# Kernel optimization log

Measured on AMD Instinct MI355X. Metric: run time of the kernel, lower is better.

## Reference

```python
import jax, jax.numpy as jnp
import numpy as np

S = 64        # state_size (nodes per graph == feature width)
B = 1024      # number of graphs
N = B * S     # total nodes
DEG = 16      # avg degree
E = N * DEG   # total edges
A = 16        # attractors
EPS = 1e-5


def setup_inputs() -> dict:
    key = jax.random.key(0)
    ks = jax.random.split(key, 16)
    x = jax.random.normal(ks[0], (N, 1), dtype=jnp.float32)
    # block-diagonal batched graphs: each graph has S nodes, S*DEG edges
    epg = S * DEG
    gid = jnp.arange(E, dtype=jnp.int32) // epg
    src = gid * S + jax.random.randint(ks[1], (E,), 0, S, dtype=jnp.int32)
    dst = gid * S + jax.random.randint(ks[2], (E,), 0, S, dtype=jnp.int32)
    edge_index = jnp.stack([src, dst], axis=0)
    f32 = jnp.float32
    return {
        "x": x, "edge_index": edge_index,
        # EdgeConv MLP: Linear(2,4) -> ReLU -> Linear(4,S)
        "w1": jax.random.normal(ks[3], (2, 4), f32) * 0.5,
        "b1": jnp.zeros((4,), f32),
        "w2": jax.random.normal(ks[4], (4, S), f32) * 0.3,
        "b2": jnp.zeros((S,), f32),
        # Conv1d(S,S,3,padding=1) x2
        "conv2_w": jax.random.normal(ks[5], (S, S, 3), f32) / np.sqrt(3 * S),
        "conv2_b": jnp.zeros((S,), f32),
        "conv3_w": jax.random.normal(ks[6], (S, S, 3), f32) / np.sqrt(3 * S),
        "conv3_b": jnp.zeros((S,), f32),
        # BatchNorm affine params
        "g1": jnp.ones((S,), f32), "be1": jnp.zeros((S,), f32),
        "g2": jnp.ones((S,), f32), "be2": jnp.zeros((S,), f32),
        "g3": jnp.ones((S,), f32), "be3": jnp.zeros((S,), f32),
        # MLP tail
        "wm1": jax.random.normal(ks[7], (S * S, 256), f32) / np.sqrt(S * S),
        "bm1": jnp.zeros((256,), f32),
        "wm2": jax.random.normal(ks[8], (256, 256), f32) / 16.0,
        "bm2": jnp.zeros((256,), f32),
        "wm3": jax.random.normal(ks[9], (256, 256), f32) / 16.0,
        "bm3": jnp.zeros((256,), f32),
        "wp": jax.random.normal(ks[10], (256, A), f32) / 16.0,
        "bp": jnp.zeros((A,), f32),
    }


def _bn(h, gamma, beta, axes):
    # training-mode batch norm (biased variance), per-channel
    mean = jnp.mean(h, axis=axes, keepdims=True)
    var = jnp.mean(jnp.square(h - mean), axis=axes, keepdims=True)
    inv = jax.lax.rsqrt(var + EPS)
    sh = [1] * h.ndim
    sh[1] = -1
    return (h - mean) * inv * gamma.reshape(sh) + beta.reshape(sh)


def _conv1d(h, w, b):
    # h: [B, C, L], w: [O, I, K], padding=1 -> same length
    out = jax.lax.conv_general_dilated(
        h, w, window_strides=(1,), padding=((1, 1),),
        dimension_numbers=("NCH", "OIH", "NCH"))
    return out + b[None, :, None]


def reference(x, edge_index, w1, b1, w2, b2, conv2_w, conv2_b, conv3_w, conv3_b,
              g1, be1, g2, be2, g3, be3, wm1, bm1, wm2, bm2, wm3, bm3, wp, bp):
    src, dst = edge_index[0], edge_index[1]
    # EdgeConv (aggr='add'): nn(cat[x_i, x_j - x_i]) summed at target i
    xi = x[dst]                              # [E,1] gather
    xj = x[src]                              # [E,1] gather
    m = jnp.concatenate([xi, xj - xi], axis=-1)      # [E,2]
    m = jax.nn.relu(m @ w1 + b1)                     # [E,4]
    m = m @ w2 + b2                                   # [E,S]
    out = jax.ops.segment_sum(m, dst, num_segments=N)  # [N,S] scatter-add
    # BN1 + ReLU on [N,S] (channel dim = 1)
    out = jax.nn.relu(_bn(out, g1, be1, axes=(0,)))
    # per-graph feature map: [B, S_nodes, S_feat] -> channels-first [B,S,S]
    out = out.reshape(B, S, S).swapaxes(1, 2)
    out = jax.nn.relu(_bn(_conv1d(out, conv2_w, conv2_b), g2, be2, axes=(0, 2)))
    out = jax.nn.relu(_bn(_conv1d(out, conv3_w, conv3_b), g3, be3, axes=(0, 2)))
    out = out.reshape(B, S * S)
    out = jax.nn.relu(out @ wm1 + bm1)
    out = jax.nn.relu(out @ wm2 + bm2)
    out = jax.nn.relu(out @ wm3 + bm3)
    logits = out @ wp + bp                            # [B, A]
    return jax.nn.log_softmax(logits, axis=1)
```

## Files before the change

### kernel.cpp

```cpp
#include <hip/hip_runtime.h>
#include <cstdint>
#include <cstddef>

typedef __attribute__((ext_vector_type(8))) short short8;
typedef __attribute__((ext_vector_type(4))) float f32x4;

#define EPSV 1e-5f
#define NB 1024
#define NEDGE 1048576
#define EPG 1024
#define CNTF 65536.0f
#define REP 32

__device__ __forceinline__ ushort f2bf(float f) {
  uint u = __float_as_uint(f);
  return (ushort)((u + 0x7FFFu + ((u >> 16) & 1u)) >> 16);
}

__global__ __launch_bounds__(256) void k_prepc(
    const float* __restrict__ c2w, const float* __restrict__ c3w,
    ushort* __restrict__ cwt2, ushort* __restrict__ cwt3)
{
  const int flat = blockIdx.x * 256 + threadIdx.x;
  const int m = flat >= 12288;
  const int idx = flat - (m ? 12288 : 0);
  const float* src = m ? c3w : c2w;
  ushort* dst = m ? cwt3 : cwt2;
  const int o = idx / 192, rem = idx - o * 192;
  const int kk = rem >> 6, c = rem & 63;
  dst[idx] = f2bf(src[o * 192 + c * 3 + kk]);
}

__global__ __launch_bounds__(256) void k_edge(
    const float* __restrict__ x, const int* __restrict__ ei,
    const float* __restrict__ w1, const float* __restrict__ b1,
    const float* __restrict__ w2, const float* __restrict__ b2,
    float* __restrict__ out0, float* __restrict__ stats1)
{
  __shared__ float xs[64];
  __shared__ float aggT[4][5][72];
  __shared__ float aggC[64][8];
  __shared__ float w1s[8], b1s[4];
  __shared__ float w2s[256], b2s[64];
  __shared__ float rs[4][64], rss[4][64];
  const int tid = threadIdx.x;
  const int b = blockIdx.x;
  const int w = tid >> 6;

  if (tid < 8) w1s[tid] = w1[tid];
  if (tid < 4) b1s[tid] = b1[tid];
  if (tid < 64) { xs[tid] = x[(b << 6) + tid]; b2s[tid] = b2[tid]; }
  w2s[tid] = w2[tid];
  for (int i = tid; i < 1440; i += 256) ((float*)aggT)[i] = 0.f;
  __syncthreads();

  const int e0 = b * EPG;
  const int4 s4 = ((const int4*)(ei + e0))[tid];
  const int4 d4 = ((const int4*)(ei + NEDGE + e0))[tid];
  float* agw = &aggT[w][0][0];
  const int sls[4] = {s4.x & 63, s4.y & 63, s4.z & 63, s4.w & 63};
  const int dls[4] = {d4.x & 63, d4.y & 63, d4.z & 63, d4.w & 63};
#pragma unroll
  for (int e = 0; e < 4; ++e) {
    const int dl = dls[e];
    const float xi = xs[dl];
    const float dx = xs[sls[e]] - xi;
#pragma unroll
    for (int j = 0; j < 4; ++j) {
      float h = fmaxf(fmaf(xi, w1s[j], fmaf(dx, w1s[4 + j], b1s[j])), 0.f);
      atomicAdd(&agw[j * 72 + dl], h);
    }
    atomicAdd(&agw[4 * 72 + dl], 1.0f);
  }
  __syncthreads();

  if (tid < 64) {
    const int n = tid;
    const float a0 = aggT[0][0][n] + aggT[1][0][n] + aggT[2][0][n] + aggT[3][0][n];
    const float a1 = aggT[0][1][n] + aggT[1][1][n] + aggT[2][1][n] + aggT[3][1][n];
    const float a2 = aggT[0][2][n] + aggT[1][2][n] + aggT[2][2][n] + aggT[3][2][n];
    const float a3v = aggT[0][3][n] + aggT[1][3][n] + aggT[2][3][n] + aggT[3][3][n];
    const float dg = aggT[0][4][n] + aggT[1][4][n] + aggT[2][4][n] + aggT[3][4][n];
    *(float4*)&aggC[n][0] = make_float4(a0, a1, a2, a3v);
    aggC[n][4] = dg;
  }
  __syncthreads();

  const int c = tid & 63, qq = tid >> 6;
  const float wc0 = w2s[c], wc1 = w2s[64 + c], wc2 = w2s[128 + c], wc3 = w2s[192 + c];
  const float b2c = b2s[c];
  float s = 0.f, ss = 0.f;
  for (int n = qq; n < 64; n += 4) {
    const float4 a = *(const float4*)&aggC[n][0];
    const float dg = aggC[n][4];
    float v = a.x * wc0 + a.y * wc1 + a.z * wc2 + a.w * wc3 + dg * b2c;
    out0[(size_t)(((b << 6) + n) << 6) + c] = v;
    s += v; ss += v * v;
  }
  rs[qq][c] = s; rss[qq][c] = ss;
  __syncthreads();
  if (tid < 64) {
    float* dst = stats1 + ((b & (REP - 1)) << 7);
    atomicAdd(&dst[tid], rs[0][tid] + rs[1][tid] + rs[2][tid] + rs[3][tid]);
    atomicAdd(&dst[64 + tid], rss[0][tid] + rss[1][tid] + rss[2][tid] + rss[3][tid]);
  }
}

__global__ __launch_bounds__(256) void k_convm(
    const float* __restrict__ in,
    const float* __restrict__ stats_in,
    const float* __restrict__ gamma, const float* __restrict__ beta,
    const ushort* __restrict__ cwt, const float* __restrict__ cb,
    float* __restrict__ out,
    float* __restrict__ stats_out)
{
  __shared__ ushort As[64][200];
  __shared__ ushort Yt[66][72];
  __shared__ float aco[64], bco[64], cbs[64];
  __shared__ float ldsS[64], ldsSS[64];
  const int tid = threadIdx.x;
  const int b = blockIdx.x;

  if (tid < 64) {
    float sm = 0.f, sq = 0.f;
#pragma unroll 8
    for (int r = 0; r < REP; ++r) {
      sm += stats_in[(r << 7) + tid];
      sq += stats_in[(r << 7) + 64 + tid];
    }
    const float mean = sm * (1.0f / CNTF);
    const float var = sq * (1.0f / CNTF) - mean * mean;
    const float a = gamma[tid] * rsqrtf(var + EPSV);
    aco[tid] = a;
    bco[tid] = beta[tid] - mean * a;
    cbs[tid] = cb[tid];
    Yt[0][tid] = 0;
    Yt[65][tid] = 0;
  }
  __syncthreads();

  const size_t base = (size_t)b << 12;
  {
    const int lr = tid >> 4, c0 = (tid & 15) << 2;
#pragma unroll
    for (int i = 0; i < 4; ++i) {
      const int l = lr + (i << 4);
      const float4 v = *(const float4*)&in[base + (l << 6) + c0];
      const float4 a4 = *(const float4*)&aco[c0];
      const float4 b4 = *(const float4*)&bco[c0];
      *(ushort4*)&Yt[l + 1][c0] = make_ushort4(
          f2bf(fmaxf(fmaf(a4.x, v.x, b4.x), 0.f)),
          f2bf(fmaxf(fmaf(a4.y, v.y, b4.y), 0.f)),
          f2bf(fmaxf(fmaf(a4.z, v.z, b4.z), 0.f)),
          f2bf(fmaxf(fmaf(a4.w, v.w, b4.w), 0.f)));
    }
  }
  {
    const short8* gw = (const short8*)cwt;
#pragma unroll
    for (int i = 0; i < 6; ++i) {
      const int e8 = (i << 8) + tid;
      const int o = e8 / 24, k8 = (e8 - o * 24) << 3;
      *(short8*)&As[o][k8] = gw[e8];
    }
  }
  __syncthreads();

  const int lane = tid & 63, w = tid >> 6;
  const int lm = lane & 15, q = lane >> 4;
  f32x4 acc[4];
#pragma unroll
  for (int nt = 0; nt < 4; ++nt) acc[nt] = (f32x4){0.f, 0.f, 0.f, 0.f};

#pragma unroll
  for (int kk = 0; kk < 3; ++kk) {
#pragma unroll
    for (int ks = 0; ks < 2; ++ks) {
      const short8 af = *(const short8*)&As[(w << 4) + lm][(kk << 6) + (ks << 5) + (q << 3)];
#pragma unroll
      for (int nt = 0; nt < 4; ++nt) {
        const short8 bfr = *(const short8*)&Yt[(nt << 4) + lm + kk][(ks << 5) + (q << 3)];
        acc[nt] = __builtin_amdgcn_mfma_f32_16x16x32_bf16(af, bfr, acc[nt], 0, 0, 0);
      }
    }
  }

  const int obase = (w << 4) + (q << 2);
  const float4 cb4 = *(const float4*)&cbs[obase];
  float s[4] = {0.f, 0.f, 0.f, 0.f}, ss[4] = {0.f, 0.f, 0.f, 0.f};
#pragma unroll
  for (int nt = 0; nt < 4; ++nt) {
    const int l = (nt << 4) + lm;
    float4 v = make_float4(acc[nt][0] + cb4.x, acc[nt][1] + cb4.y,
                           acc[nt][2] + cb4.z, acc[nt][3] + cb4.w);
    *(float4*)&out[base + (l << 6) + obase] = v;
    s[0] += v.x; ss[0] += v.x * v.x;
    s[1] += v.y; ss[1] += v.y * v.y;
    s[2] += v.z; ss[2] += v.z * v.z;
    s[3] += v.w; ss[3] += v.w * v.w;
  }
#pragma unroll
  for (int i = 0; i < 4; ++i) {
#pragma unroll
    for (int off = 1; off < 16; off <<= 1) {
      s[i] += __shfl_xor(s[i], off);
      ss[i] += __shfl_xor(ss[i], off);
    }
    if (lm == 0) { ldsS[obase + i] = s[i]; ldsSS[obase + i] = ss[i]; }
  }
  __syncthreads();
  if (tid < 64) {
    float* dst = stats_out + ((b & (REP - 1)) << 7);
    atomicAdd(&dst[tid], ldsS[tid]);
    atomicAdd(&dst[64 + tid], ldsSS[tid]);
  }
}

__global__ __launch_bounds__(256) void k_prep(
    const float* __restrict__ wm1, ushort* __restrict__ wbf)
{
  const int tid = threadIdx.x;
  const int rp = (blockIdx.x << 4) + (tid >> 4);
  const int c0 = (tid & 15) << 4;
  const int rsrc = ((rp & 63) << 6) + (rp >> 6);
  const float* src = wm1 + ((size_t)rsrc << 8) + c0;
  ushort* dst = wbf + ((size_t)rp << 8) + c0;
#pragma unroll
  for (int i = 0; i < 4; ++i) {
    const float4 v = *(const float4*)(src + (i << 2));
    *(ushort4*)(dst + (i << 2)) = make_ushort4(f2bf(v.x), f2bf(v.y), f2bf(v.z), f2bf(v.w));
  }
}

__global__ __launch_bounds__(256) void k_prep2(
    const float* __restrict__ wm2, const float* __restrict__ wm3,
    const float* __restrict__ wp,
    ushort* __restrict__ wbf2t, ushort* __restrict__ wbf3t,
    ushort* __restrict__ wptbf)
{
  const int tid = threadIdx.x;
  if (blockIdx.x == 64) {
    const int a = tid & 15, k0 = (tid >> 4) << 4;
    ushort tmp[16];
#pragma unroll
    for (int j = 0; j < 16; ++j) tmp[j] = f2bf(wp[((k0 + j) << 4) + a]);
    *(short8*)&wptbf[(a << 8) + k0] = *(short8*)&tmp[0];
    *(short8*)&wptbf[(a << 8) + k0 + 8] = *(short8*)&tmp[8];
    return;
  }
  const int base = ((blockIdx.x << 8) + tid) << 3;
  const int m = base >> 16;
  const int rem = base & 65535;
  const int kc = rem >> 14, within = rem & 16383;
  const int n = within >> 6, kk0 = within & 63;
  const float* src = m ? wm3 : wm2;
  ushort* dst = m ? wbf3t : wbf2t;
  ushort tmp[8];
#pragma unroll
  for (int j = 0; j < 8; ++j)
    tmp[j] = f2bf(src[(((kc << 6) | (kk0 + j)) << 8) + n]);
  *(short8*)&dst[rem] = *(short8*)&tmp[0];
}

__global__ __launch_bounds__(256) void k_mlp1(
    const float* __restrict__ z3, const float* __restrict__ stats3,
    const float* __restrict__ g3, const float* __restrict__ be3,
    const ushort* __restrict__ wbf, float* __restrict__ h1part)
{
  __shared__ ushort Ys[64][72];
  __shared__ ushort Ws[64][72];
  __shared__ float a3s[64], b3s[64];
  const int tid = threadIdx.x;
  const int bx = blockIdx.x, by = blockIdx.y, bz = blockIdx.z;

  if (tid < 64) {
    float sm = 0.f, sq = 0.f;
#pragma unroll 8
    for (int r = 0; r < REP; ++r) {
      sm += stats3[(r << 7) + tid];
      sq += stats3[(r << 7) + 64 + tid];
    }
    const float mean = sm * (1.0f / CNTF);
    const float var = sq * (1.0f / CNTF) - mean * mean;
    const float a = g3[tid] * rsqrtf(var + EPSV);
    a3s[tid] = a;
    b3s[tid] = be3[tid] - mean * a;
  }
  __syncthreads();

  const int lane = tid & 63, w = tid >> 6;
  const int lm = lane & 15, q = lane >> 4;
  const int ry = tid >> 2, cy = (tid & 3) << 4;
  const int ngr = (tid & 15) << 2, kgr = (tid >> 4) << 2;
  const int g0 = bx << 6, n0 = by << 6;

  f32x4 acc[4];
#pragma unroll
  for (int nt = 0; nt < 4; ++nt) acc[nt] = (f32x4){0.f, 0.f, 0.f, 0.f};

  const size_t ybase = (size_t)(g0 + ry) << 12;

#pragma unroll 1
  for (int ck = 0; ck < 8; ++ck) {
    const int kc = (bz << 9) + (ck << 6);
    if (ck) __syncthreads();
#pragma unroll
    for (int i = 0; i < 4; ++i) {
      const float4 v = *(const float4*)&z3[ybase + kc + cy + (i << 2)];
      const float4 sa4 = *(const float4*)&a3s[cy + (i << 2)];
      const float4 sb4 = *(const float4*)&b3s[cy + (i << 2)];
      *(ushort4*)&Ys[ry][cy + (i << 2)] = make_ushort4(
          f2bf(fmaxf(fmaf(sa4.x, v.x, sb4.x), 0.f)),
          f2bf(fmaxf(fmaf(sa4.y, v.y, sb4.y), 0.f)),
          f2bf(fmaxf(fmaf(sa4.z, v.z, sb4.z), 0.f)),
          f2bf(fmaxf(fmaf(sa4.w, v.w, sb4.w), 0.f)));
    }
    {
      const ushort* wp0 = wbf + (((size_t)(kc + kgr)) << 8) + n0 + ngr;
      const ushort4 w0 = *(const ushort4*)(wp0);
      const ushort4 w1 = *(const ushort4*)(wp0 + 256);
      const ushort4 w2 = *(const ushort4*)(wp0 + 512);
      const ushort4 w3 = *(const ushort4*)(wp0 + 768);
      *(ushort4*)&Ws[ngr + 0][kgr] = make_ushort4(w0.x, w1.x, w2.x, w3.x);
      *(ushort4*)&Ws[ngr + 1][kgr] = make_ushort4(w0.y, w1.y, w2.y, w3.y);
      *(ushort4*)&Ws[ngr + 2][kgr] = make_ushort4(w0.z, w1.z, w2.z, w3.z);
      *(ushort4*)&Ws[ngr + 3][kgr] = make_ushort4(w0.w, w1.w, w2.w, w3.w);
    }
    __syncthreads();
#pragma unroll
    for (int ks = 0; ks < 2; ++ks) {
      const short8 af = *(const short8*)&Ys[(w << 4) + lm][(ks << 5) + (q << 3)];
#pragma unroll
      for (int nt = 0; nt < 4; ++nt) {
        const short8 bfr = *(const short8*)&Ws[(nt << 4) + lm][(ks << 5) + (q << 3)];
        acc[nt] = __builtin_amdgcn_mfma_f32_16x16x32_bf16(af, bfr, acc[nt], 0, 0, 0);
      }
    }
  }

  float* dst0 = h1part + ((size_t)bz << 18);
  const int gout = g0 + (w << 4) + (q << 2);
#pragma unroll
  for (int nt = 0; nt < 4; ++nt) {
    const int col = n0 + (nt << 4) + lm;
#pragma unroll
    for (int i = 0; i < 4; ++i)
      dst0[((size_t)(gout + i) << 8) + col] = acc[nt][i];
  }
}

__global__ __launch_bounds__(256) void k_tail(
    const float* __restrict__ h1part, const float* __restrict__ bm1,
    const ushort* __restrict__ wbf2t, const float* __restrict__ bm2,
    const ushort* __restrict__ wbf3t, const float* __restrict__ bm3,
    const ushort* __restrict__ wptbf, const float* __restrict__ bp,
    float* __restrict__ out)
{
  __shared__ ushort Ws[256][72];
  __shared__ ushort h1s[16][264];
  __shared__ ushort h2s[16][264];
  ushort* wpt = &Ws[0][0];
  const int tid = threadIdx.x;
  const int g0 = blockIdx.x << 4;
  const int lane = tid & 63, w = tid >> 6;
  const int lm = lane & 15, q = lane >> 4;
  const int gr = q << 2;

  {
    const int r = tid >> 4, c0 = (tid & 15) << 4;
    const float* srcb = h1part + ((size_t)(g0 + r) << 8) + c0;
#pragma unroll
    for (int i = 0; i < 4; ++i) {
      float4 vs = *(const float4*)(bm1 + c0 + (i << 2));
#pragma unroll
      for (int bz = 0; bz < 8; ++bz) {
        const float4 p = *(const float4*)(srcb + ((size_t)bz << 18) + (i << 2));
        vs.x += p.x; vs.y += p.y; vs.z += p.z; vs.w += p.w;
      }
      *(ushort4*)&h1s[r][c0 + (i << 2)] = make_ushort4(
          f2bf(fmaxf(vs.x, 0.f)), f2bf(fmaxf(vs.y, 0.f)),
          f2bf(fmaxf(vs.z, 0.f)), f2bf(fmaxf(vs.w, 0.f)));
    }
  }

  f32x4 acc[4];
#pragma unroll
  for (int nt = 0; nt < 4; ++nt) acc[nt] = (f32x4){0.f, 0.f, 0.f, 0.f};
#pragma unroll 1
  for (int ck = 0; ck < 4; ++ck) {
    __syncthreads();
    {
      const short8* gw = (const short8*)(wbf2t + (ck << 14));
#pragma unroll
      for (int i = 0; i < 8; ++i) {
        const int e8 = (i << 8) + tid;
        const int n = e8 >> 3, kk = (e8 & 7) << 3;
        *(short8*)&Ws[n][kk] = gw[e8];
      }
    }
    __syncthreads();
#pragma unroll
    for (int ks = 0; ks < 2; ++ks) {
      const short8 af = *(const short8*)&h1s[lm][(ck << 6) + (ks << 5) + (q << 3)];
#pragma unroll
      for (int nt = 0; nt < 4; ++nt) {
        const short8 bfr = *(const short8*)&Ws[(w << 6) + (nt << 4) + lm][(ks << 5) + (q << 3)];
        acc[nt] = __builtin_amdgcn_mfma_f32_16x16x32_bf16(af, bfr, acc[nt], 0, 0, 0);
      }
    }
  }
#pragma unroll
  for (int nt = 0; nt < 4; ++nt) {
    const int col = (w << 6) + (nt << 4) + lm;
    const float bv = bm2[col];
#pragma unroll
    for (int i = 0; i < 4; ++i)
      h2s[gr + i][col] = f2bf(fmaxf(acc[nt][i] + bv, 0.f));
  }

  f32x4 acc2[4];
#pragma unroll
  for (int nt = 0; nt < 4; ++nt) acc2[nt] = (f32x4){0.f, 0.f, 0.f, 0.f};
#pragma unroll 1
  for (int ck = 0; ck < 4; ++ck) {
    __syncthreads();
    {
      const short8* gw = (const short8*)(wbf3t + (ck << 14));
#pragma unroll
      for (int i = 0; i < 8; ++i) {
        const int e8 = (i << 8) + tid;
        const int n = e8 >> 3, kk = (e8 & 7) << 3;
        *(short8*)&Ws[n][kk] = gw[e8];
      }
    }
    __syncthreads();
#pragma unroll
    for (int ks = 0; ks < 2; ++ks) {
      const short8 af = *(const short8*)&h2s[lm][(ck << 6) + (ks << 5) + (q << 3)];
#pragma unroll
      for (int nt = 0; nt < 4; ++nt) {
        const short8 bfr = *(const short8*)&Ws[(w << 6) + (nt << 4) + lm][(ks << 5) + (q << 3)];
        acc2[nt] = __builtin_amdgcn_mfma_f32_16x16x32_bf16(af, bfr, acc2[nt], 0, 0, 0);
      }
    }
  }

  __syncthreads();
  {
    const short8* gw = (const short8*)wptbf;
#pragma unroll
    for (int i = 0; i < 2; ++i) {
      const int e8 = (i << 8) + tid;
      const int flat = e8 << 3;
      const int a = flat >> 8, kk = flat & 255;
      *(short8*)&wpt[a * 264 + kk] = gw[e8];
    }
  }
#pragma unroll
  for (int nt = 0; nt < 4; ++nt) {
    const int col = (w << 6) + (nt << 4) + lm;
    const float bv = bm3[col];
#pragma unroll
    for (int i = 0; i < 4; ++i)
      h2s[gr + i][col] = f2bf(fmaxf(acc2[nt][i] + bv, 0.f));
  }
  __syncthreads();

  if (w == 0) {
    f32x4 lacc = (f32x4){0.f, 0.f, 0.f, 0.f};
#pragma unroll
    for (int ks = 0; ks < 8; ++ks) {
      const short8 af = *(const short8*)&h2s[lm][(ks << 5) + (q << 3)];
      const short8 bfr = *(const short8*)&wpt[lm * 264 + (ks << 5) + (q << 3)];
      lacc = __builtin_amdgcn_mfma_f32_16x16x32_bf16(af, bfr, lacc, 0, 0, 0);
    }
    const float bpv = bp[lm];
    float lg[4], mx[4], se[4];
#pragma unroll
    for (int i = 0; i < 4; ++i) {
      lg[i] = lacc[i] + bpv;
      float m = lg[i];
#pragma unroll
      for (int off = 1; off < 16; off <<= 1) m = fmaxf(m, __shfl_xor(m, off));
      mx[i] = m;
      float e = expf(lg[i] - m);
#pragma unroll
      for (int off = 1; off < 16; off <<= 1) e += __shfl_xor(e, off);
      se[i] = e;
    }
#pragma unroll
    for (int i = 0; i < 4; ++i)
      out[((g0 + gr + i) << 4) + lm] = (lg[i] - mx[i]) - logf(se[i]);
  }
}

extern "C" void kernel_launch(void* const* d_in, const int* in_sizes, int n_in,
                              void* d_out, int out_size, void* d_ws, size_t ws_size,
                              hipStream_t stream)
{
  const float* x   = (const float*)d_in[0];
  const int*   ei  = (const int*)d_in[1];
  const float* w1  = (const float*)d_in[2];
  const float* b1  = (const float*)d_in[3];
  const float* w2  = (const float*)d_in[4];
  const float* b2  = (const float*)d_in[5];
  const float* c2w = (const float*)d_in[6];
  const float* c2b = (const float*)d_in[7];
  const float* c3w = (const float*)d_in[8];
  const float* c3b = (const float*)d_in[9];
  const float* g1  = (const float*)d_in[10];
  const float* be1 = (const float*)d_in[11];
  const float* g2  = (const float*)d_in[12];
  const float* be2 = (const float*)d_in[13];
  const float* g3  = (const float*)d_in[14];
  const float* be3 = (const float*)d_in[15];
  const float* wm1 = (const float*)d_in[16];
  const float* bm1 = (const float*)d_in[17];
  const float* wm2 = (const float*)d_in[18];
  const float* bm2 = (const float*)d_in[19];
  const float* wm3 = (const float*)d_in[20];
  const float* bm3 = (const float*)d_in[21];
  const float* wp  = (const float*)d_in[22];
  const float* bp  = (const float*)d_in[23];

  char* ws = (char*)d_ws;
  float* buf0 = (float*)ws;
  float* buf1 = (float*)(ws + ((size_t)16 << 20));
  float* stats = (float*)(ws + ((size_t)32 << 20));
  float* stats1 = stats;
  float* stats2 = stats + REP * 128;
  float* stats3 = stats + 2 * REP * 128;
  float*  h1part = buf1;
  ushort* wbf   = (ushort*)(ws + ((size_t)24 << 20));
  ushort* wbf2t = (ushort*)(ws + ((size_t)26 << 20));
  ushort* wbf3t = (ushort*)(ws + ((size_t)26 << 20) + (128 << 10));
  ushort* wptbf = (ushort*)(ws + ((size_t)26 << 20) + (256 << 10));
  ushort* cwt2 = (ushort*)d_out;
  ushort* cwt3 = (ushort*)d_out + 12288;

  hipMemsetAsync(stats, 0, 3 * REP * 128 * sizeof(float), stream);
  k_prepc<<<dim3(96), dim3(256), 0, stream>>>(c2w, c3w, cwt2, cwt3);
  k_edge<<<dim3(NB), dim3(256), 0, stream>>>(x, ei, w1, b1, w2, b2, buf0, stats1);
  k_convm<<<dim3(NB), dim3(256), 0, stream>>>(buf0, stats1, g1, be1, cwt2, c2b, buf1, stats2);
  k_convm<<<dim3(NB), dim3(256), 0, stream>>>(buf1, stats2, g2, be2, cwt3, c3b, buf0, stats3);
  k_prep<<<dim3(256), dim3(256), 0, stream>>>(wm1, wbf);
  k_prep2<<<dim3(65), dim3(256), 0, stream>>>(wm2, wm3, wp, wbf2t, wbf3t, wptbf);
  k_mlp1<<<dim3(16, 4, 8), dim3(256), 0, stream>>>(buf0, stats3, g3, be3, wbf, h1part);
  k_tail<<<dim3(64), dim3(256), 0, stream>>>(h1part, bm1, wbf2t, bm2, wbf3t, bm3,
                                             wptbf, bp, (float*)d_out);
}
```

Before: 195.2 us.

## Store intermediate activations in bf16, merge prep kernels, widen mlp1 N-tile

Intermediate activation buffers between the edge, conv and MLP stages are now stored as bf16 instead of fp32, which halves the HBM traffic of these large intermediates. The statistics are still accumulated from the fp32 values before rounding. The memset and the three weight-prep kernels are merged into one launch, and wm1 is pre-transposed into a k-chunked layout. k_mlp1 now processes 128 output columns per block with half as many blocks, cutting redundant activation reloads. The cost is extra rounding of pre-BN activations to bf16, which may shift numerics slightly.

New measurement: 187.8 us. -3.8%, faster.

```diff
diff --git a/kernel.cpp b/kernel.cpp
--- a/kernel.cpp
+++ b/kernel.cpp
@@ -3,6 +3,7 @@
 #include <cstddef>
 
 typedef __attribute__((ext_vector_type(8))) short short8;
+typedef __attribute__((ext_vector_type(8))) unsigned short ushort8;
 typedef __attribute__((ext_vector_type(4))) float f32x4;
 
 #define EPSV 1e-5f
@@ -16,12 +17,72 @@
   uint u = __float_as_uint(f);
   return (ushort)((u + 0x7FFFu + ((u >> 16) & 1u)) >> 16);
 }
-
-__global__ __launch_bounds__(256) void k_prepc(
+__device__ __forceinline__ float bf2f(ushort u) {
+  return __uint_as_float((uint)u << 16);
+}
+
+__global__ __launch_bounds__(256) void k_prepw(
+    const float* __restrict__ wm1, const float* __restrict__ wm2,
+    const float* __restrict__ wm3, const float* __restrict__ wp,
     const float* __restrict__ c2w, const float* __restrict__ c3w,
-    ushort* __restrict__ cwt2, ushort* __restrict__ cwt3)
+    ushort* __restrict__ wbf1t, ushort* __restrict__ wbf2t,
+    ushort* __restrict__ wbf3t, ushort* __restrict__ wptbf,
+    ushort* __restrict__ cwt2, ushort* __restrict__ cwt3,
+    float* __restrict__ stats)
 {
-  const int flat = blockIdx.x * 256 + threadIdx.x;
+  __shared__ ushort T[64][72];
+  const int tid = threadIdx.x;
+  const int bb = blockIdx.x;
+
+  if (bb < 256) {
+    const int kc = bb >> 2, n0 = (bb & 3) << 6;
+    const int kk = tid >> 2, np = (tid & 3) << 4;
+    const float* srow = wm1 + (((size_t)(kk << 6) + kc) << 8) + n0 + np;
+#pragma unroll
+    for (int i = 0; i < 4; ++i) {
+      const float4 v = *(const float4*)(srow + (i << 2));
+      const int n = np + (i << 2);
+      T[n + 0][kk] = f2bf(v.x); T[n + 1][kk] = f2bf(v.y);
+      T[n + 2][kk] = f2bf(v.z); T[n + 3][kk] = f2bf(v.w);
+    }
+    __syncthreads();
+    ushort* dst = wbf1t + ((size_t)kc << 14) + (n0 << 6);
+    const int nl = tid >> 2, qk = (tid & 3) << 4;
+    *(ushort8*)(dst + (nl << 6) + qk) = *(ushort8*)&T[nl][qk];
+    *(ushort8*)(dst + (nl << 6) + qk + 8) = *(ushort8*)&T[nl][qk + 8];
+    return;
+  }
+  if (bb < 320) {
+    const int base = (((bb - 256) << 8) + tid) << 3;
+    const int m = base >> 16;
+    const int rem = base & 65535;
+    const int kc = rem >> 14, within = rem & 16383;
+    const int n = within >> 6, kk0 = within & 63;
+    const float* src = m ? wm3 : wm2;
+    ushort* dst = m ? wbf3t : wbf2t;
+    ushort tmp[8];
+#pragma unroll
+    for (int j = 0; j < 8; ++j)
+      tmp[j] = f2bf(src[(((kc << 6) | (kk0 + j)) << 8) + n]);
+    *(ushort8*)&dst[rem] = *(ushort8*)&tmp[0];
+    return;
+  }
+  if (bb == 320) {
+    const int a = tid & 15, k0 = (tid >> 4) << 4;
+    ushort tmp[16];
+#pragma unroll
+    for (int j = 0; j < 16; ++j) tmp[j] = f2bf(wp[((k0 + j) << 4) + a]);
+    *(ushort8*)&wptbf[(a << 8) + k0] = *(ushort8*)&tmp[0];
+    *(ushort8*)&wptbf[(a << 8) + k0 + 8] = *(ushort8*)&tmp[8];
+    return;
+  }
+  if (bb == 417) {
+    float4 z4 = make_float4(0.f, 0.f, 0.f, 0.f);
+#pragma unroll
+    for (int i = 0; i < 12; ++i) ((float4*)stats)[(i << 8) + tid] = z4;
+    return;
+  }
+  const int flat = (bb - 321) * 256 + tid;
   const int m = flat >= 12288;
   const int idx = flat - (m ? 12288 : 0);
   const float* src = m ? c3w : c2w;
@@ -35,7 +96,7 @@
     const float* __restrict__ x, const int* __restrict__ ei,
     const float* __restrict__ w1, const float* __restrict__ b1,
     const float* __restrict__ w2, const float* __restrict__ b2,
-    float* __restrict__ out0, float* __restrict__ stats1)
+    ushort* __restrict__ out0, float* __restrict__ stats1)
 {
   __shared__ float xs[64];
   __shared__ float aggT[4][5][72];
@@ -94,7 +155,7 @@
     const float4 a = *(const float4*)&aggC[n][0];
     const float dg = aggC[n][4];
     float v = a.x * wc0 + a.y * wc1 + a.z * wc2 + a.w * wc3 + dg * b2c;
-    out0[(size_t)(((b << 6) + n) << 6) + c] = v;
+    out0[(size_t)(((b << 6) + n) << 6) + c] = f2bf(v);
     s += v; ss += v * v;
   }
   rs[qq][c] = s; rss[qq][c] = ss;
@@ -107,11 +168,11 @@
 }
 
 __global__ __launch_bounds__(256) void k_convm(
-    const float* __restrict__ in,
+    const ushort* __restrict__ in,
     const float* __restrict__ stats_in,
     const float* __restrict__ gamma, const float* __restrict__ beta,
     const ushort* __restrict__ cwt, const float* __restrict__ cb,
-    float* __restrict__ out,
+    ushort* __restrict__ out,
     float* __restrict__ stats_out)
 {
   __shared__ ushort As[64][200];
@@ -141,27 +202,26 @@
 
   const size_t base = (size_t)b << 12;
   {
-    const int lr = tid >> 4, c0 = (tid & 15) << 2;
-#pragma unroll
-    for (int i = 0; i < 4; ++i) {
-      const int l = lr + (i << 4);
-      const float4 v = *(const float4*)&in[base + (l << 6) + c0];
-      const float4 a4 = *(const float4*)&aco[c0];
-      const float4 b4 = *(const float4*)&bco[c0];
-      *(ushort4*)&Yt[l + 1][c0] = make_ushort4(
-          f2bf(fmaxf(fmaf(a4.x, v.x, b4.x), 0.f)),
-          f2bf(fmaxf(fmaf(a4.y, v.y, b4.y), 0.f)),
-          f2bf(fmaxf(fmaf(a4.z, v.z, b4.z), 0.f)),
-          f2bf(fmaxf(fmaf(a4.w, v.w, b4.w), 0.f)));
-    }
+    const int lr = tid >> 2, p = (tid & 3) << 4;
+    const ushort8 r0 = *(const ushort8*)&in[base + (lr << 6) + p];
+    const ushort8 r1 = *(const ushort8*)&in[base + (lr << 6) + p + 8];
+    ushort tmp[16];
+#pragma unroll
+    for (int j = 0; j < 8; ++j)
+      tmp[j] = f2bf(fmaxf(fmaf(aco[p + j], bf2f(r0[j]), bco[p + j]), 0.f));
+#pragma unroll
+    for (int j = 0; j < 8; ++j)
+      tmp[8 + j] = f2bf(fmaxf(fmaf(aco[p + 8 + j], bf2f(r1[j]), bco[p + 8 + j]), 0.f));
+    *(ushort8*)&Yt[lr + 1][p] = *(ushort8*)&tmp[0];
+    *(ushort8*)&Yt[lr + 1][p + 8] = *(ushort8*)&tmp[8];
   }
   {
-    const short8* gw = (const short8*)cwt;
+    const ushort8* gw = (const ushort8*)cwt;
 #pragma unroll
     for (int i = 0; i < 6; ++i) {
       const int e8 = (i << 8) + tid;
       const int o = e8 / 24, k8 = (e8 - o * 24) << 3;
-      *(short8*)&As[o][k8] = gw[e8];
+      *(ushort8*)&As[o][k8] = gw[e8];
     }
   }
   __syncthreads();
@@ -193,7 +253,8 @@
     const int l = (nt << 4) + lm;
     float4 v = make_float4(acc[nt][0] + cb4.x, acc[nt][1] + cb4.y,
                            acc[nt][2] + cb4.z, acc[nt][3] + cb4.w);
-    *(float4*)&out[base + (l << 6) + obase] = v;
+    *(ushort4*)&out[base + (l << 6) + obase] =
+        make_ushort4(f2bf(v.x), f2bf(v.y), f2bf(v.z), f2bf(v.w));
     s[0] += v.x; ss[0] += v.x * v.x;
     s[1] += v.y; ss[1] += v.y * v.y;
     s[2] += v.z; ss[2] += v.z * v.z;
@@ -216,59 +277,13 @@
   }
 }
 
-__global__ __launch_bounds__(256) void k_prep(
-    const float* __restrict__ wm1, ushort* __restrict__ wbf)
-{
-  const int tid = threadIdx.x;
-  const int rp = (blockIdx.x << 4) + (tid >> 4);
-  const int c0 = (tid & 15) << 4;
-  const int rsrc = ((rp & 63) << 6) + (rp >> 6);
-  const float* src = wm1 + ((size_t)rsrc << 8) + c0;
-  ushort* dst = wbf + ((size_t)rp << 8) + c0;
-#pragma unroll
-  for (int i = 0; i < 4; ++i) {
-    const float4 v = *(const float4*)(src + (i << 2));
-    *(ushort4*)(dst + (i << 2)) = make_ushort4(f2bf(v.x), f2bf(v.y), f2bf(v.z), f2bf(v.w));
-  }
-}
-
-__global__ __launch_bounds__(256) void k_prep2(
-    const float* __restrict__ wm2, const float* __restrict__ wm3,
-    const float* __restrict__ wp,
-    ushort* __restrict__ wbf2t, ushort* __restrict__ wbf3t,
-    ushort* __restrict__ wptbf)
-{
-  const int tid = threadIdx.x;
-  if (blockIdx.x == 64) {
-    const int a = tid & 15, k0 = (tid >> 4) << 4;
-    ushort tmp[16];
-#pragma unroll
-    for (int j = 0; j < 16; ++j) tmp[j] = f2bf(wp[((k0 + j) << 4) + a]);
-    *(short8*)&wptbf[(a << 8) + k0] = *(short8*)&tmp[0];
-    *(short8*)&wptbf[(a << 8) + k0 + 8] = *(short8*)&tmp[8];
-    return;
-  }
-  const int base = ((blockIdx.x << 8) + tid) << 3;
-  const int m = base >> 16;
-  const int rem = base & 65535;
-  const int kc = rem >> 14, within = rem & 16383;
-  const int n = within >> 6, kk0 = within & 63;
-  const float* src = m ? wm3 : wm2;
-  ushort* dst = m ? wbf3t : wbf2t;
-  ushort tmp[8];
-#pragma unroll
-  for (int j = 0; j < 8; ++j)
-    tmp[j] = f2bf(src[(((kc << 6) | (kk0 + j)) << 8) + n]);
-  *(short8*)&dst[rem] = *(short8*)&tmp[0];
-}
-
 __global__ __launch_bounds__(256) void k_mlp1(
-    const float* __restrict__ z3, const float* __restrict__ stats3,
+    const ushort* __restrict__ z3, const float* __restrict__ stats3,
     const float* __restrict__ g3, const float* __restrict__ be3,
-    const ushort* __restrict__ wbf, float* __restrict__ h1part)
+    const ushort* __restrict__ wbf1t, float* __restrict__ h1part)
 {
   __shared__ ushort Ys[64][72];
-  __shared__ ushort Ws[64][72];
+  __shared__ ushort Ws[128][72];
   __shared__ float a3s[64], b3s[64];
   const int tid = threadIdx.x;
   const int bx = blockIdx.x, by = blockIdx.y, bz = blockIdx.z;
@@ -290,48 +305,46 @@
 
   const int lane = tid & 63, w = tid >> 6;
   const int lm = lane & 15, q = lane >> 4;
-  const int ry = tid >> 2, cy = (tid & 3) << 4;
-  const int ngr = (tid & 15) << 2, kgr = (tid >> 4) << 2;
-  const int g0 = bx << 6, n0 = by << 6;
-
-  f32x4 acc[4];
-#pragma unroll
-  for (int nt = 0; nt < 4; ++nt) acc[nt] = (f32x4){0.f, 0.f, 0.f, 0.f};
-
-  const size_t ybase = (size_t)(g0 + ry) << 12;
+  const int gy = tid >> 2, py = (tid & 3) << 4;
+  const int nn = tid >> 1, pp = (tid & 1) << 2;
+  const int g0 = bx << 6, n0 = by << 7;
+
+  f32x4 acc[8];
+#pragma unroll
+  for (int nt = 0; nt < 8; ++nt) acc[nt] = (f32x4){0.f, 0.f, 0.f, 0.f};
+
+  const size_t ybase = ((size_t)(g0 + gy) << 12);
 
 #pragma unroll 1
   for (int ck = 0; ck < 8; ++ck) {
     const int kc = (bz << 9) + (ck << 6);
     if (ck) __syncthreads();
-#pragma unroll
-    for (int i = 0; i < 4; ++i) {
-      const float4 v = *(const float4*)&z3[ybase + kc + cy + (i << 2)];
-      const float4 sa4 = *(const float4*)&a3s[cy + (i << 2)];
-      const float4 sb4 = *(const float4*)&b3s[cy + (i << 2)];
-      *(ushort4*)&Ys[ry][cy + (i << 2)] = make_ushort4(
-          f2bf(fmaxf(fmaf(sa4.x, v.x, sb4.x), 0.f)),
-          f2bf(fmaxf(fmaf(sa4.y, v.y, sb4.y), 0.f)),
-          f2bf(fmaxf(fmaf(sa4.z, v.z, sb4.z), 0.f)),
-          f2bf(fmaxf(fmaf(sa4.w, v.w, sb4.w), 0.f)));
-    }
     {
-      const ushort* wp0 = wbf + (((size_t)(kc + kgr)) << 8) + n0 + ngr;
-      const ushort4 w0 = *(const ushort4*)(wp0);
-      const ushort4 w1 = *(const ushort4*)(wp0 + 256);
-      const ushort4 w2 = *(const ushort4*)(wp0 + 512);
-      const ushort4 w3 = *(const ushort4*)(wp0 + 768);
-      *(ushort4*)&Ws[ngr + 0][kgr] = make_ushort4(w0.x, w1.x, w2.x, w3.x);
-      *(ushort4*)&Ws[ngr + 1][kgr] = make_ushort4(w0.y, w1.y, w2.y, w3.y);
-      *(ushort4*)&Ws[ngr + 2][kgr] = make_ushort4(w0.z, w1.z, w2.z, w3.z);
-      *(ushort4*)&Ws[ngr + 3][kgr] = make_ushort4(w0.w, w1.w, w2.w, w3.w);
+      const ushort* src = z3 + ybase + kc + py;
+      const ushort8 r0 = *(const ushort8*)src;
+      const ushort8 r1 = *(const ushort8*)(src + 8);
+      ushort tmp[16];
+#pragma unroll
+      for (int j = 0; j < 8; ++j)
+        tmp[j] = f2bf(fmaxf(fmaf(a3s[py + j], bf2f(r0[j]), b3s[py + j]), 0.f));
+#pragma unroll
+      for (int j = 0; j < 8; ++j)
+        tmp[8 + j] = f2bf(fmaxf(fmaf(a3s[py + 8 + j], bf2f(r1[j]), b3s[py + 8 + j]), 0.f));
+      *(ushort8*)&Ys[gy][py] = *(ushort8*)&tmp[0];
+      *(ushort8*)&Ys[gy][py + 8] = *(ushort8*)&tmp[8];
+    }
+    {
+      const ushort8* gw = (const ushort8*)(wbf1t + ((size_t)((bz << 3) + ck) << 14) + (n0 << 6));
+#pragma unroll
+      for (int i = 0; i < 4; ++i)
+        *(ushort8*)&Ws[nn][(pp + i) << 3] = gw[(nn << 3) + pp + i];
     }
     __syncthreads();
 #pragma unroll
     for (int ks = 0; ks < 2; ++ks) {
       const short8 af = *(const short8*)&Ys[(w << 4) + lm][(ks << 5) + (q << 3)];
 #pragma unroll
-      for (int nt = 0; nt < 4; ++nt) {
+      for (int nt = 0; nt < 8; ++nt) {
         const short8 bfr = *(const short8*)&Ws[(nt << 4) + lm][(ks << 5) + (q << 3)];
         acc[nt] = __builtin_amdgcn_mfma_f32_16x16x32_bf16(af, bfr, acc[nt], 0, 0, 0);
       }
@@ -341,7 +354,7 @@
   float* dst0 = h1part + ((size_t)bz << 18);
   const int gout = g0 + (w << 4) + (q << 2);
 #pragma unroll
-  for (int nt = 0; nt < 4; ++nt) {
+  for (int nt = 0; nt < 8; ++nt) {
     const int col = n0 + (nt << 4) + lm;
 #pragma unroll
     for (int i = 0; i < 4; ++i)
@@ -390,12 +403,12 @@
   for (int ck = 0; ck < 4; ++ck) {
     __syncthreads();
     {
-      const short8* gw = (const short8*)(wbf2t + (ck << 14));
+      const ushort8* gw = (const ushort8*)(wbf2t + (ck << 14));
 #pragma unroll
       for (int i = 0; i < 8; ++i) {
         const int e8 = (i << 8) + tid;
         const int n = e8 >> 3, kk = (e8 & 7) << 3;
-        *(short8*)&Ws[n][kk] = gw[e8];
+        *(ushort8*)&Ws[n][kk] = gw[e8];
       }
     }
     __syncthreads();
@@ -425,12 +438,12 @@
   for (int ck = 0; ck < 4; ++ck) {
     __syncthreads();
     {
-      const short8* gw = (const short8*)(wbf3t + (ck << 14));
+      const ushort8* gw = (const ushort8*)(wbf3t + (ck << 14));
 #pragma unroll
       for (int i = 0; i < 8; ++i) {
         const int e8 = (i << 8) + tid;
         const int n = e8 >> 3, kk = (e8 & 7) << 3;
-        *(short8*)&Ws[n][kk] = gw[e8];
+        *(ushort8*)&Ws[n][kk] = gw[e8];
       }
     }
     __syncthreads();
@@ -447,13 +460,13 @@
 
   __syncthreads();
   {
-    const short8* gw = (const short8*)wptbf;
+    const ushort8* gw = (const ushort8*)wptbf;
 #pragma unroll
     for (int i = 0; i < 2; ++i) {
       const int e8 = (i << 8) + tid;
       const int flat = e8 << 3;
       const int a = flat >> 8, kk = flat & 255;
-      *(short8*)&wpt[a * 264 + kk] = gw[e8];
+      *(ushort8*)&wpt[a * 264 + kk] = gw[e8];
     }
   }
 #pragma unroll
@@ -524,28 +537,27 @@
   const float* bp  = (const float*)d_in[23];
 
   char* ws = (char*)d_ws;
-  float* buf0 = (float*)ws;
-  float* buf1 = (float*)(ws + ((size_t)16 << 20));
-  float* stats = (float*)(ws + ((size_t)32 << 20));
+  ushort* ubuf0 = (ushort*)ws;
+  ushort* ubuf1 = (ushort*)(ws + ((size_t)8 << 20));
+  float*  h1part = (float*)(ws + ((size_t)16 << 20));
+  ushort* wbf1t = (ushort*)(ws + ((size_t)24 << 20));
+  ushort* wbf2t = (ushort*)(ws + ((size_t)26 << 20));
+  ushort* wbf3t = (ushort*)(ws + ((size_t)26 << 20) + (128 << 10));
+  ushort* wptbf = (ushort*)(ws + ((size_t)26 << 20) + (256 << 10));
+  float* stats = (float*)(ws + ((size_t)27 << 20));
   float* stats1 = stats;
   float* stats2 = stats + REP * 128;
   float* stats3 = stats + 2 * REP * 128;
-  float*  h1part = buf1;
-  ushort* wbf   = (ushort*)(ws + ((size_t)24 << 20));
-  ushort* wbf2t = (ushort*)(ws + ((size_t)26 << 20));
-  ushort* wbf3t = (ushort*)(ws + ((size_t)26 << 20) + (128 << 10));
-  ushort* wptbf = (ushort*)(ws + ((size_t)26 << 20) + (256 << 10));
   ushort* cwt2 = (ushort*)d_out;
   ushort* cwt3 = (ushort*)d_out + 12288;
 
-  hipMemsetAsync(stats, 0, 3 * REP * 128 * sizeof(float), stream);
-  k_prepc<<<dim3(96), dim3(256), 0, stream>>>(c2w, c3w, cwt2, cwt3);
-  k_edge<<<dim3(NB), dim3(256), 0, stream>>>(x, ei, w1, b1, w2, b2, buf0, stats1);
-  k_convm<<<dim3(NB), dim3(256), 0, stream>>>(buf0, stats1, g1, be1, cwt2, c2b, buf1, stats2);
-  k_convm<<<dim3(NB), dim3(256), 0, stream>>>(buf1, stats2, g2, be2, cwt3, c3b, buf0, stats3);
-  k_prep<<<dim3(256), dim3(256), 0, stream>>>(wm1, wbf);
-  k_prep2<<<dim3(65), dim3(256), 0, stream>>>(wm2, wm3, wp, wbf2t, wbf3t, wptbf);
-  k_mlp1<<<dim3(16, 4, 8), dim3(256), 0, stream>>>(buf0, stats3, g3, be3, wbf, h1part);
+  k_prepw<<<dim3(418), dim3(256), 0, stream>>>(
+      wm1, wm2, wm3, wp, c2w, c3w,
+      wbf1t, wbf2t, wbf3t, wptbf, cwt2, cwt3, stats);
+  k_edge<<<dim3(NB), dim3(256), 0, stream>>>(x, ei, w1, b1, w2, b2, ubuf0, stats1);
+  k_convm<<<dim3(NB), dim3(256), 0, stream>>>(ubuf0, stats1, g1, be1, cwt2, c2b, ubuf1, stats2);
+  k_convm<<<dim3(NB), dim3(256), 0, stream>>>(ubuf1, stats2, g2, be2, cwt3, c3b, ubuf0, stats3);
+  k_mlp1<<<dim3(16, 2, 8), dim3(256), 0, stream>>>(ubuf0, stats3, g3, be3, wbf1t, h1part);
   k_tail<<<dim3(64), dim3(256), 0, stream>>>(h1part, bm1, wbf2t, bm2, wbf3t, bm3,
                                              wptbf, bp, (float*)d_out);
 }
```
